# Optimization experiments

Measured on AMD Instinct MI355X. Metric: run time of the kernel, lower is better.

## Reference

```python
import jax, jax.numpy as jnp
import numpy as np

D_MODEL = 1024
N_HEAD = 16
D_HEAD = D_MODEL // N_HEAD


def setup_inputs() -> dict:
    key = jax.random.key(0)
    ks = jax.random.split(key, 12)
    L, B, M = 2048, 2, 2048
    s = 1.0 / np.sqrt(D_MODEL)
    return {
        "q": jax.random.normal(ks[0], (L, B, D_MODEL), jnp.float32),
        "kv": jax.random.normal(ks[1], (L, B, D_MODEL), jnp.float32),
        "mem": jax.random.normal(ks[2], (M, B, D_MODEL), jnp.float32),
        "w_q": jax.random.normal(ks[3], (D_MODEL, D_MODEL), jnp.float32) * s,
        "b_q": jnp.zeros((D_MODEL,), jnp.float32),
        "w_k": jax.random.normal(ks[4], (D_MODEL, D_MODEL), jnp.float32) * s,
        "b_k": jnp.zeros((D_MODEL,), jnp.float32),
        "w_v": jax.random.normal(ks[5], (D_MODEL, D_MODEL), jnp.float32) * s,
        "b_v": jnp.zeros((D_MODEL,), jnp.float32),
        "w_c": jax.random.normal(ks[6], (D_MODEL, D_MODEL), jnp.float32) * s,
        "b_c": jnp.zeros((D_MODEL,), jnp.float32),
    }


def reference(q, kv, mem, w_q, b_q, w_k, b_k, w_v, b_v, w_c, b_c):
    # c: [L+M, B, D]
    c = jnp.concatenate([mem, kv], axis=0)
    L, B, _ = q.shape
    J = c.shape[0]
    # linear projections (torch Linear: x @ W^T + b)
    qh = (q @ w_q.T + b_q).reshape(L, B, N_HEAD, D_HEAD)
    kh = (c @ w_k.T + b_k).reshape(J, B, N_HEAD, D_HEAD)
    vh = (c @ w_v.T + b_v).reshape(J, B, N_HEAD, D_HEAD)
    # attention scores [i, j, b, n]
    score = jnp.einsum("ibnd,jbnd->ijbn", qh, kh) / np.sqrt(D_HEAD).astype(np.float32)
    prob = jax.nn.softmax(score, axis=1)
    vec = jnp.einsum("ijbn,jbnd->ibnd", prob, vh).reshape(L, B, D_MODEL)
    return vec @ w_c.T + b_c
```

## Files before the change

### kernel.cpp

```cpp
#include <hip/hip_runtime.h>


using short8 = __attribute__((ext_vector_type(8))) short;
using f32x4  = __attribute__((ext_vector_type(4))) float;

#define DEV __device__ __forceinline__

DEV unsigned short f2bf(float f) {
  union { float f; unsigned int u; } x; x.f = f;
  unsigned int r = x.u + 0x7FFFu + ((x.u >> 16) & 1u);
  return (unsigned short)(r >> 16);
}

DEV unsigned int cvtpk(float lo, float hi) {
  unsigned int r;
  asm("v_cvt_pk_bf16_f32 %0, %1, %2" : "=v"(r) : "v"(lo), "v"(hi));
  return r;
}

DEV float max3f(float a, float b, float c) {
  float d;
  asm("v_max3_f32 %0, %1, %2, %3" : "=v"(d) : "v"(a), "v"(b), "v"(c));
  return d;
}

DEV void gload_lds16(const unsigned short* g, unsigned short* l) {
  __builtin_amdgcn_global_load_lds(
      (const __attribute__((address_space(1))) unsigned int*)g,
      (__attribute__((address_space(3))) unsigned int*)l, 16, 0, 0);
}

#define BARRIER_RAW()                      \
  do {                                     \
    __builtin_amdgcn_sched_barrier(0);     \
    __builtin_amdgcn_s_barrier();          \
    __builtin_amdgcn_sched_barrier(0);     \
  } while (0)

__global__ __launch_bounds__(256) void convert_all(
    const float* __restrict__ q, const float* __restrict__ mem_,
    const float* __restrict__ kv, const float* __restrict__ wq,
    const float* __restrict__ wk, const float* __restrict__ wv,
    const float* __restrict__ wc, unsigned short* __restrict__ a_bf,
    unsigned short* __restrict__ c_bf, unsigned short* __restrict__ w_bf) {
  size_t u = (size_t)blockIdx.x * 256 + threadIdx.x;
  const float* src;
  unsigned short* dst;
  if (u < 524288u)        { src = q    + u * 8;                dst = a_bf + u * 8; }
  else if (u < 1048576u)  { src = mem_ + (u - 524288u) * 8;    dst = c_bf + (u - 524288u) * 8; }
  else if (u < 1572864u)  { src = kv   + (u - 1048576u) * 8;   dst = c_bf + 4194304u + (u - 1048576u) * 8; }
  else if (u < 1703936u)  { src = wq   + (u - 1572864u) * 8;   dst = w_bf + (u - 1572864u) * 8; }
  else if (u < 1835008u)  { src = wk   + (u - 1703936u) * 8;   dst = w_bf + 1048576u + (u - 1703936u) * 8; }
  else if (u < 1966080u)  { src = wv   + (u - 1835008u) * 8;   dst = w_bf + 2097152u + (u - 1835008u) * 8; }
  else                    { src = wc   + (u - 1966080u) * 8;   dst = w_bf + 3145728u + (u - 1966080u) * 8; }
  float4 v0 = ((const float4*)src)[0];
  float4 v1 = ((const float4*)src)[1];
  union { unsigned short us[8]; uint4 v; } o;
  o.us[0] = f2bf(v0.x); o.us[1] = f2bf(v0.y); o.us[2] = f2bf(v0.z); o.us[3] = f2bf(v0.w);
  o.us[4] = f2bf(v1.x); o.us[5] = f2bf(v1.y); o.us[6] = f2bf(v1.z); o.us[7] = f2bf(v1.w);
  *(uint4*)dst = o.v;
}

template <int MODE>
__global__ __launch_bounds__(256, 2) void gemm_bt(
    const unsigned short* __restrict__ A, const unsigned short* __restrict__ Bw,
    const float* __restrict__ bias, void* __restrict__ outp) {
  __shared__ __align__(16) unsigned short lA[128 * 64];
  __shared__ __align__(16) unsigned short lB[128 * 64];
  const int tid = threadIdx.x;
  const int lane = tid & 63;
  const int w = tid >> 6;
  const int wr = w >> 1, wcn = w & 1;
  const int tm = blockIdx.x * 128;
  const int tn = blockIdx.y * 128;

  const int srow = lane >> 3;
  const int scol = ((lane & 7) ^ srow) * 8;
  const unsigned short* aptr = A + (size_t)(tm + 32 * w + srow) * 1024 + scol;
  const unsigned short* bptr = Bw + (size_t)(tn + 32 * w + srow) * 1024 + scol;
  unsigned short* lAw = &lA[(32 * w) * 64];
  unsigned short* lBw = &lB[(32 * w) * 64];

  const f32x4 zero = {0.f, 0.f, 0.f, 0.f};
  f32x4 acc[4][4];
#pragma unroll
  for (int i = 0; i < 4; ++i)
#pragma unroll
    for (int j = 0; j < 4; ++j) acc[i][j] = zero;

  for (int kb = 0; kb < 16; ++kb) {
    const int ko = kb * 64;
#pragma unroll
    for (int c = 0; c < 4; ++c) {
      gload_lds16(aptr + ko + c * 8 * 1024, lAw + c * 8 * 64);
      gload_lds16(bptr + ko + c * 8 * 1024, lBw + c * 8 * 64);
    }
    __syncthreads();
#pragma unroll
    for (int kk = 0; kk < 2; ++kk) {
      short8 af[4], bfr[4];
#pragma unroll
      for (int mi = 0; mi < 4; ++mi) {
        int r = 64 * wr + 16 * mi + (lane & 15);
        int slot = (kk * 4 + (lane >> 4)) ^ (r & 7);
        af[mi] = *(const short8*)&lA[r * 64 + slot * 8];
      }
#pragma unroll
      for (int ni = 0; ni < 4; ++ni) {
        int r = 64 * wcn + 16 * ni + (lane & 15);
        int slot = (kk * 4 + (lane >> 4)) ^ (r & 7);
        bfr[ni] = *(const short8*)&lB[r * 64 + slot * 8];
      }
#pragma unroll
      for (int mi = 0; mi < 4; ++mi)
#pragma unroll
        for (int ni = 0; ni < 4; ++ni)
          acc[mi][ni] = __builtin_amdgcn_mfma_f32_16x16x32_bf16(
              af[mi], bfr[ni], acc[mi][ni], 0, 0, 0);
    }
    __syncthreads();
  }

  const int g4 = (lane >> 4) * 4;
  const int c0 = lane & 15;
#pragma unroll
  for (int mi = 0; mi < 4; ++mi) {
#pragma unroll
    for (int ni = 0; ni < 4; ++ni) {
      const int colt = tn + 64 * wcn + 16 * ni + c0;
      const float bv = bias[colt];
#pragma unroll
      for (int j = 0; j < 4; ++j) {
        const int rowt = tm + 64 * wr + 16 * mi + g4 + j;
        const float v = acc[mi][ni][j] + bv;
        if constexpr (MODE == 0) {
          ((float*)outp)[(size_t)rowt * 1024 + colt] = v;
        } else if constexpr (MODE == 1) {
          const int i = rowt >> 1, b = rowt & 1, n = colt >> 6, d = colt & 63;
          ((unsigned short*)outp)[(((size_t)(b * 16 + n) * 2048 + i) << 6) + d] =
              f2bf(v * 0.1803368801111f);
        } else if constexpr (MODE == 2) {
          const int jj = rowt >> 1, b = rowt & 1, n = colt >> 6, d = colt & 63;
          ((unsigned short*)outp)[(((size_t)(b * 16 + n) * 4096 + jj) << 6) + d] = f2bf(v);
        } else {
          const int jj = rowt >> 1, b = rowt & 1, n = colt >> 6, d = colt & 63;
          const int j6 = jj & 63;
          const int pos = (j6 & 3) | (((j6 >> 4) & 1) << 2) | (((j6 >> 2) & 3) << 3) |
                          (((j6 >> 5) & 1) << 5);
          ((unsigned short*)outp)[((size_t)(b * 16 + n) * 64 + d) * 4096 + (jj & ~63) + pos] =
              f2bf(v);
        }
      }
    }
  }
}

__global__ __launch_bounds__(256, 2) void attn_kernel(
    const unsigned short* __restrict__ qh, const unsigned short* __restrict__ kh,
    const unsigned short* __restrict__ vt, unsigned short* __restrict__ vec) {
  __shared__ __align__(16) unsigned short kl[2][2][64 * 64];
  __shared__ __align__(16) unsigned short vl[2][2][64 * 64];
  const int tid = threadIdx.x;
  const int lane = tid & 63;
  const int w = tid >> 6;
  const int g = lane >> 4;
  const int l4 = lane & 15;
  const int f = blockIdx.x;
  const int head = (f & 7) * 4 + ((f >> 3) & 3);
  const int qt = f >> 5;
  const int b = head >> 4, n = head & 15;
  const unsigned short* qbase = qh + ((size_t)head * 2048 + qt * 128 + 32 * w) * 64;
  const unsigned short* kbase = kh + (size_t)head * 4096 * 64;
  const unsigned short* vbase = vt + (size_t)head * 64 * 4096;

  short8 qf[2][2];
#pragma unroll
  for (int mi = 0; mi < 2; ++mi)
#pragma unroll
    for (int kk = 0; kk < 2; ++kk)
      qf[mi][kk] = *(const short8*)&qbase[(16 * mi + l4) * 64 + kk * 32 + g * 8];

  const f32x4 zero = {0.f, 0.f, 0.f, 0.f};
  f32x4 oacc[2][4];
#pragma unroll
  for (int mi = 0; mi < 2; ++mi)
#pragma unroll
    for (int nd = 0; nd < 4; ++nd) oacc[mi][nd] = zero;
  float mrow[2] = {-3.0e38f, -3.0e38f};
  float lsum[2] = {0.f, 0.f};

  const int srow = lane >> 3;
  const int scol = ((lane & 7) ^ srow) * 8;
  const unsigned short* kp = kbase + (size_t)(16 * w + srow) * 64 + scol;
  const unsigned short* vp = vbase + (size_t)(16 * w + srow) * 4096 + scol;

  auto stage_pair = [&](int jp, int bufi) {
#pragma unroll
    for (int sub = 0; sub < 2; ++sub) {
      gload_lds16(kp + (size_t)jp * 8192 + sub * 4096,
                  &kl[bufi][sub][(16 * w) * 64]);
      gload_lds16(kp + (size_t)jp * 8192 + sub * 4096 + 8 * 64,
                  &kl[bufi][sub][(16 * w + 8) * 64]);
      gload_lds16(vp + jp * 128 + sub * 64, &vl[bufi][sub][(16 * w) * 64]);
      gload_lds16(vp + jp * 128 + sub * 64 + 8 * 4096,
                  &vl[bufi][sub][(16 * w + 8) * 64]);
    }
  };

  auto subtile = [&](const unsigned short* kbuf, const unsigned short* vbuf) {
    f32x4 s[2][4];
#pragma unroll
    for (int mi = 0; mi < 2; ++mi)
#pragma unroll
      for (int nj = 0; nj < 4; ++nj) s[mi][nj] = zero;
    __builtin_amdgcn_s_setprio(1);
#pragma unroll
    for (int kk = 0; kk < 2; ++kk) {
      short8 bk[4];
#pragma unroll
      for (int nj = 0; nj < 4; ++nj) {
        int r = 16 * nj + l4;
        int slot = (kk * 4 + g) ^ (r & 7);
        bk[nj] = *(const short8*)&kbuf[r * 64 + slot * 8];
      }
#pragma unroll
      for (int mi = 0; mi < 2; ++mi)
#pragma unroll
        for (int nj = 0; nj < 4; ++nj)
          s[mi][nj] = __builtin_amdgcn_mfma_f32_16x16x32_bf16(bk[nj], qf[mi][kk], s[mi][nj], 0, 0, 0);
    }
    __builtin_amdgcn_s_setprio(0);

    float pm[2];
#pragma unroll
    for (int mi = 0; mi < 2; ++mi) {
      float t0 = max3f(s[mi][0][0], s[mi][0][1], s[mi][0][2]);
      float t1 = max3f(s[mi][0][3], s[mi][1][0], s[mi][1][1]);
      float t2 = max3f(s[mi][1][2], s[mi][1][3], s[mi][2][0]);
      float t3 = max3f(s[mi][2][1], s[mi][2][2], s[mi][2][3]);
      float t4 = max3f(s[mi][3][0], s[mi][3][1], s[mi][3][2]);
      float p5 = max3f(t0, t1, t2);
      p5 = max3f(p5, t3, t4);
      pm[mi] = fmaxf(p5, s[mi][3][3]);
    }
    float pj = fmaxf(pm[0], pm[1]);
    pj = fmaxf(pj, __shfl_xor(pj, 16));
    pj = fmaxf(pj, __shfl_xor(pj, 32));
    if (!__all(pj <= fminf(mrow[0], mrow[1]) + 8.f)) {
#pragma unroll
      for (int mi = 0; mi < 2; ++mi) {
        const float mnew = fmaxf(mrow[mi], pj);
        const float sc = __builtin_amdgcn_exp2f(mrow[mi] - mnew);
        mrow[mi] = mnew;
        lsum[mi] *= sc;
#pragma unroll
        for (int reg = 0; reg < 4; ++reg) {
          const float scr = __shfl(sc, 4 * g + reg);
#pragma unroll
          for (int nd = 0; nd < 4; ++nd) oacc[mi][nd][reg] *= scr;
        }
      }
    }

    short8 pa[2][2];
#pragma unroll
    for (int mi = 0; mi < 2; ++mi) {
      const float m = mrow[mi];
      float rs = 0.f;
#pragma unroll
      for (int nj = 0; nj < 4; ++nj)
#pragma unroll
        for (int reg = 0; reg < 4; ++reg) {
          const float p = __builtin_amdgcn_exp2f(s[mi][nj][reg] - m);
          s[mi][nj][reg] = p;
          rs += p;
        }
      lsum[mi] += rs;
#pragma unroll
      for (int kk2 = 0; kk2 < 2; ++kk2) {
        union { unsigned int u[4]; short8 v; } t;
#pragma unroll
        for (int wd = 0; wd < 4; ++wd) {
          const int nj = (wd >> 1) + 2 * kk2;
          const int r0 = (wd & 1) * 2;
          t.u[wd] = cvtpk(s[mi][nj][r0], s[mi][nj][r0 + 1]);
        }
        pa[mi][kk2] = t.v;
      }
    }

    __builtin_amdgcn_s_setprio(1);
#pragma unroll
    for (int kk2 = 0; kk2 < 2; ++kk2) {
      short8 bv4[4];
#pragma unroll
      for (int nd = 0; nd < 4; ++nd) {
        const int r = 16 * nd + l4;
        const int blk = (g + 4 * kk2) ^ (r & 7);
        bv4[nd] = *(const short8*)&vbuf[r * 64 + blk * 8];
      }
#pragma unroll
      for (int mi = 0; mi < 2; ++mi)
#pragma unroll
        for (int nd = 0; nd < 4; ++nd)
          oacc[mi][nd] = __builtin_amdgcn_mfma_f32_16x16x32_bf16(pa[mi][kk2], bv4[nd], oacc[mi][nd], 0, 0, 0);
    }
    __builtin_amdgcn_s_setprio(0);
  };

  stage_pair(0, 0);
  asm volatile("s_waitcnt vmcnt(0)" ::: "memory");
  BARRIER_RAW();

  for (int t2 = 0; t2 < 16; ++t2) {
    stage_pair(2 * t2 + 1, 1);
    subtile(kl[0][0], vl[0][0]);
    subtile(kl[0][1], vl[0][1]);
    asm volatile("s_waitcnt vmcnt(0)" ::: "memory");
    BARRIER_RAW();
    if (t2 < 15) stage_pair(2 * t2 + 2, 0);
    subtile(kl[1][0], vl[1][0]);
    subtile(kl[1][1], vl[1][1]);
    if (t2 < 15) {
      asm volatile("s_waitcnt vmcnt(0)" ::: "memory");
      BARRIER_RAW();
    }
  }

#pragma unroll
  for (int mi = 0; mi < 2; ++mi) {
    float l = lsum[mi];
    l += __shfl_xor(l, 16);
    l += __shfl_xor(l, 32);
#pragma unroll
    for (int reg = 0; reg < 4; ++reg) {
      const float lr = __shfl(l, 4 * g + reg);
      const float inv = 1.f / lr;
      const int i = qt * 128 + 32 * w + 16 * mi + 4 * g + reg;
#pragma unroll
      for (int nd = 0; nd < 4; ++nd) {
        const int d = 16 * nd + l4;
        vec[(size_t)(i * 2 + b) * 1024 + n * 64 + d] = f2bf(oacc[mi][nd][reg] * inv);
      }
    }
  }
}

extern "C" void kernel_launch(void* const* d_in, const int* in_sizes, int n_in,
                              void* d_out, int out_size, void* d_ws, size_t ws_size,
                              hipStream_t stream) {
  (void)in_sizes; (void)n_in; (void)out_size; (void)ws_size;
  const float* q    = (const float*)d_in[0];
  const float* kv   = (const float*)d_in[1];
  const float* mem_ = (const float*)d_in[2];
  const float* wq   = (const float*)d_in[3];
  const float* bq   = (const float*)d_in[4];
  const float* wk   = (const float*)d_in[5];
  const float* bk   = (const float*)d_in[6];
  const float* wv   = (const float*)d_in[7];
  const float* bv   = (const float*)d_in[8];
  const float* wc   = (const float*)d_in[9];
  const float* bc   = (const float*)d_in[10];

  char* ws = (char*)d_ws;
  unsigned short* w_bf = (unsigned short*)(ws);
  unsigned short* a_bf = (unsigned short*)(ws + (8ull << 20));
  unsigned short* c_bf = (unsigned short*)(ws + (16ull << 20));
  unsigned short* qhb  = (unsigned short*)(ws + (32ull << 20));
  unsigned short* khb  = (unsigned short*)(ws + (40ull << 20));
  unsigned short* vtb  = (unsigned short*)(ws + (56ull << 20));
  unsigned short* vecb = a_bf;

  convert_all<<<8192, 256, 0, stream>>>(q, mem_, kv, wq, wk, wv, wc, a_bf, c_bf, w_bf);
  gemm_bt<1><<<dim3(32, 8), 256, 0, stream>>>(a_bf, w_bf,                bq, qhb);
  gemm_bt<2><<<dim3(64, 8), 256, 0, stream>>>(c_bf, w_bf + (1u << 20),   bk, khb);
  gemm_bt<3><<<dim3(64, 8), 256, 0, stream>>>(c_bf, w_bf + (2u << 20),   bv, vtb);
  attn_kernel<<<512, 256, 0, stream>>>(qhb, khb, vtb, vecb);
  gemm_bt<0><<<dim3(32, 8), 256, 0, stream>>>(vecb, w_bf + (3u << 20),   bc, d_out);
}
```

Before: 189.6 us.

## Split attention over two key halves and merge partials in a combine kernel

The attention kernel now splits the 4096 keys of each head into two halves, doubling the grid to 1024 blocks and raising the launch-bounds occupancy target to 4 blocks per CU with half the LDS staging. Each block writes a normalized partial output plus its row max and row sum. A new combine kernel rescales and merges the two partials into the final layout. This is meant to improve latency hiding and CU occupancy, at the cost of an extra launch and extra global traffic for the partial outputs.

```diff
diff --git a/kernel.cpp b/kernel.cpp
--- a/kernel.cpp
+++ b/kernel.cpp
@@ -10,6 +10,12 @@
   union { float f; unsigned int u; } x; x.f = f;
   unsigned int r = x.u + 0x7FFFu + ((x.u >> 16) & 1u);
   return (unsigned short)(r >> 16);
+}
+
+DEV float bf2f(unsigned short u) {
+  union { unsigned int u; float f; } x;
+  x.u = ((unsigned int)u) << 16;
+  return x.f;
 }
 
 DEV unsigned int cvtpk(float lo, float hi) {
@@ -155,20 +161,21 @@
   }
 }
 
-__global__ __launch_bounds__(256, 2) void attn_kernel(
+__global__ __launch_bounds__(256, 4) void attn_kernel(
     const unsigned short* __restrict__ qh, const unsigned short* __restrict__ kh,
-    const unsigned short* __restrict__ vt, unsigned short* __restrict__ vec) {
-  __shared__ __align__(16) unsigned short kl[2][2][64 * 64];
-  __shared__ __align__(16) unsigned short vl[2][2][64 * 64];
+    const unsigned short* __restrict__ vt, unsigned short* __restrict__ po,
+    float2* __restrict__ ml) {
+  __shared__ __align__(16) unsigned short kl[2][64 * 64];
+  __shared__ __align__(16) unsigned short vl[2][64 * 64];
   const int tid = threadIdx.x;
   const int lane = tid & 63;
   const int w = tid >> 6;
   const int g = lane >> 4;
   const int l4 = lane & 15;
   const int f = blockIdx.x;
-  const int head = (f & 7) * 4 + ((f >> 3) & 3);
-  const int qt = f >> 5;
-  const int b = head >> 4, n = head & 15;
+  const int head = (f & 7) * 4 + (f >> 8);
+  const int qt = (f >> 3) & 15;
+  const int half = (f >> 7) & 1;
   const unsigned short* qbase = qh + ((size_t)head * 2048 + qt * 128 + 32 * w) * 64;
   const unsigned short* kbase = kh + (size_t)head * 4096 * 64;
   const unsigned short* vbase = vt + (size_t)head * 64 * 4096;
@@ -193,18 +200,14 @@
   const int scol = ((lane & 7) ^ srow) * 8;
   const unsigned short* kp = kbase + (size_t)(16 * w + srow) * 64 + scol;
   const unsigned short* vp = vbase + (size_t)(16 * w + srow) * 4096 + scol;
-
-  auto stage_pair = [&](int jp, int bufi) {
-#pragma unroll
-    for (int sub = 0; sub < 2; ++sub) {
-      gload_lds16(kp + (size_t)jp * 8192 + sub * 4096,
-                  &kl[bufi][sub][(16 * w) * 64]);
-      gload_lds16(kp + (size_t)jp * 8192 + sub * 4096 + 8 * 64,
-                  &kl[bufi][sub][(16 * w + 8) * 64]);
-      gload_lds16(vp + jp * 128 + sub * 64, &vl[bufi][sub][(16 * w) * 64]);
-      gload_lds16(vp + jp * 128 + sub * 64 + 8 * 4096,
-                  &vl[bufi][sub][(16 * w + 8) * 64]);
-    }
+  const int stbase = half * 32;
+
+  auto stage = [&](int st, int bufi) {
+    const size_t jt = (size_t)(stbase + st);
+    gload_lds16(kp + jt * 4096,            &kl[bufi][(16 * w) * 64]);
+    gload_lds16(kp + jt * 4096 + 8 * 64,   &kl[bufi][(16 * w + 8) * 64]);
+    gload_lds16(vp + jt * 64,              &vl[bufi][(16 * w) * 64]);
+    gload_lds16(vp + jt * 64 + 8 * 4096,   &vl[bufi][(16 * w + 8) * 64]);
   };
 
   auto subtile = [&](const unsigned short* kbuf, const unsigned short* vbuf) {
@@ -308,19 +311,17 @@
     __builtin_amdgcn_s_setprio(0);
   };
 
-  stage_pair(0, 0);
+  stage(0, 0);
   asm volatile("s_waitcnt vmcnt(0)" ::: "memory");
   BARRIER_RAW();
 
   for (int t2 = 0; t2 < 16; ++t2) {
-    stage_pair(2 * t2 + 1, 1);
-    subtile(kl[0][0], vl[0][0]);
-    subtile(kl[0][1], vl[0][1]);
+    stage(2 * t2 + 1, 1);
+    subtile(kl[0], vl[0]);
     asm volatile("s_waitcnt vmcnt(0)" ::: "memory");
     BARRIER_RAW();
-    if (t2 < 15) stage_pair(2 * t2 + 2, 0);
-    subtile(kl[1][0], vl[1][0]);
-    subtile(kl[1][1], vl[1][1]);
+    if (t2 < 15) stage(2 * t2 + 2, 0);
+    subtile(kl[1], vl[1]);
     if (t2 < 15) {
       asm volatile("s_waitcnt vmcnt(0)" ::: "memory");
       BARRIER_RAW();
@@ -332,18 +333,48 @@
     float l = lsum[mi];
     l += __shfl_xor(l, 16);
     l += __shfl_xor(l, 32);
+    const int rowbase = head * 2048 + qt * 128 + 32 * w + 16 * mi;
+    if (g == 0)
+      ml[(size_t)half * 65536 + rowbase + l4] = make_float2(mrow[mi], l);
 #pragma unroll
     for (int reg = 0; reg < 4; ++reg) {
       const float lr = __shfl(l, 4 * g + reg);
       const float inv = 1.f / lr;
-      const int i = qt * 128 + 32 * w + 16 * mi + 4 * g + reg;
+      const size_t row = rowbase + 4 * g + reg;
 #pragma unroll
       for (int nd = 0; nd < 4; ++nd) {
         const int d = 16 * nd + l4;
-        vec[(size_t)(i * 2 + b) * 1024 + n * 64 + d] = f2bf(oacc[mi][nd][reg] * inv);
+        po[(size_t)half * 4194304 + row * 64 + d] = f2bf(oacc[mi][nd][reg] * inv);
       }
     }
   }
+}
+
+__global__ __launch_bounds__(256) void attn_combine(
+    const unsigned short* __restrict__ po, const float2* __restrict__ ml,
+    unsigned short* __restrict__ vec) {
+  const size_t u = (size_t)blockIdx.x * 256 + threadIdx.x;
+  const size_t row = u >> 3;
+  const int d0 = (int)(u & 7) * 8;
+  const int head = (int)(row >> 11);
+  const int i = (int)(row & 2047);
+  const int b = head >> 4, n = head & 15;
+
+  const float2 m0 = ml[row];
+  const float2 m1 = ml[65536 + row];
+  const float m = fmaxf(m0.x, m1.x);
+  const float w0 = m0.y * __builtin_amdgcn_exp2f(m0.x - m);
+  const float w1 = m1.y * __builtin_amdgcn_exp2f(m1.x - m);
+  const float inv = 1.f / (w0 + w1);
+  const float a0 = w0 * inv, a1 = w1 * inv;
+
+  union { uint4 v; unsigned short us[8]; } p0, p1, o;
+  p0.v = *(const uint4*)&po[row * 64 + d0];
+  p1.v = *(const uint4*)&po[4194304 + row * 64 + d0];
+#pragma unroll
+  for (int k = 0; k < 8; ++k)
+    o.us[k] = f2bf(bf2f(p0.us[k]) * a0 + bf2f(p1.us[k]) * a1);
+  *(uint4*)&vec[(size_t)(i * 2 + b) * 1024 + n * 64 + d0] = o.v;
 }
 
 extern "C" void kernel_launch(void* const* d_in, const int* in_sizes, int n_in,
@@ -370,11 +401,14 @@
   unsigned short* khb  = (unsigned short*)(ws + (40ull << 20));
   unsigned short* vtb  = (unsigned short*)(ws + (56ull << 20));
   unsigned short* vecb = a_bf;
+  unsigned short* po   = c_bf;
+  float2*         ml   = (float2*)ws;
 
   convert_all<<<8192, 256, 0, stream>>>(q, mem_, kv, wq, wk, wv, wc, a_bf, c_bf, w_bf);
   gemm_bt<1><<<dim3(32, 8), 256, 0, stream>>>(a_bf, w_bf,                bq, qhb);
   gemm_bt<2><<<dim3(64, 8), 256, 0, stream>>>(c_bf, w_bf + (1u << 20),   bk, khb);
   gemm_bt<3><<<dim3(64, 8), 256, 0, stream>>>(c_bf, w_bf + (2u << 20),   bv, vtb);
-  attn_kernel<<<512, 256, 0, stream>>>(qhb, khb, vtb, vecb);
+  attn_kernel<<<1024, 256, 0, stream>>>(qhb, khb, vtb, po, ml);
+  attn_combine<<<2048, 256, 0, stream>>>(po, ml, vecb);
   gemm_bt<0><<<dim3(32, 8), 256, 0, stream>>>(vecb, w_bf + (3u << 20),   bc, d_out);
 }
```

Measured after the change: 204.4 us. 1.08x slower.

## Merge K/V projection launches and interleave two QK^T subtiles in attention

Applied to the files above, without the earlier changes.

Replaces the separate K and V projection GEMM launches with a single gemm_kv kernel on a 64x16 grid, where the y index selects the weight, bias and output layout. This removes one launch and the tail of a 512-block grid. The attention loop now issues both QK^T MFMA subtiles before their softmax and PV stages, so the second subtile's matrix work can overlap the first's exp/softmax, at the cost of more live registers. The row-sum reduction is also reshaped into a pairwise tree to shorten the dependency chain.

```diff
diff --git a/kernel.cpp b/kernel.cpp
--- a/kernel.cpp
+++ b/kernel.cpp
@@ -135,20 +135,101 @@
         const float v = acc[mi][ni][j] + bv;
         if constexpr (MODE == 0) {
           ((float*)outp)[(size_t)rowt * 1024 + colt] = v;
-        } else if constexpr (MODE == 1) {
+        } else {
           const int i = rowt >> 1, b = rowt & 1, n = colt >> 6, d = colt & 63;
           ((unsigned short*)outp)[(((size_t)(b * 16 + n) * 2048 + i) << 6) + d] =
               f2bf(v * 0.1803368801111f);
-        } else if constexpr (MODE == 2) {
-          const int jj = rowt >> 1, b = rowt & 1, n = colt >> 6, d = colt & 63;
-          ((unsigned short*)outp)[(((size_t)(b * 16 + n) * 4096 + jj) << 6) + d] = f2bf(v);
+        }
+      }
+    }
+  }
+}
+
+__global__ __launch_bounds__(256, 2) void gemm_kv(
+    const unsigned short* __restrict__ A, const unsigned short* __restrict__ wk,
+    const unsigned short* __restrict__ wv, const float* __restrict__ bk,
+    const float* __restrict__ bv, unsigned short* __restrict__ ko,
+    unsigned short* __restrict__ vo) {
+  __shared__ __align__(16) unsigned short lA[128 * 64];
+  __shared__ __align__(16) unsigned short lB[128 * 64];
+  const int tid = threadIdx.x;
+  const int lane = tid & 63;
+  const int w = tid >> 6;
+  const int wr = w >> 1, wcn = w & 1;
+  const int tm = blockIdx.x * 128;
+  const int yy = blockIdx.y;
+  const bool isV = yy >= 8;
+  const int tn = (yy & 7) * 128;
+  const unsigned short* Bw = isV ? wv : wk;
+  const float* bias = isV ? bv : bk;
+
+  const int srow = lane >> 3;
+  const int scol = ((lane & 7) ^ srow) * 8;
+  const unsigned short* aptr = A + (size_t)(tm + 32 * w + srow) * 1024 + scol;
+  const unsigned short* bptr = Bw + (size_t)(tn + 32 * w + srow) * 1024 + scol;
+  unsigned short* lAw = &lA[(32 * w) * 64];
+  unsigned short* lBw = &lB[(32 * w) * 64];
+
+  const f32x4 zero = {0.f, 0.f, 0.f, 0.f};
+  f32x4 acc[4][4];
+#pragma unroll
+  for (int i = 0; i < 4; ++i)
+#pragma unroll
+    for (int j = 0; j < 4; ++j) acc[i][j] = zero;
+
+  for (int kb = 0; kb < 16; ++kb) {
+    const int ko_ = kb * 64;
+#pragma unroll
+    for (int c = 0; c < 4; ++c) {
+      gload_lds16(aptr + ko_ + c * 8 * 1024, lAw + c * 8 * 64);
+      gload_lds16(bptr + ko_ + c * 8 * 1024, lBw + c * 8 * 64);
+    }
+    __syncthreads();
+#pragma unroll
+    for (int kk = 0; kk < 2; ++kk) {
+      short8 af[4], bfr[4];
+#pragma unroll
+      for (int mi = 0; mi < 4; ++mi) {
+        int r = 64 * wr + 16 * mi + (lane & 15);
+        int slot = (kk * 4 + (lane >> 4)) ^ (r & 7);
+        af[mi] = *(const short8*)&lA[r * 64 + slot * 8];
+      }
+#pragma unroll
+      for (int ni = 0; ni < 4; ++ni) {
+        int r = 64 * wcn + 16 * ni + (lane & 15);
+        int slot = (kk * 4 + (lane >> 4)) ^ (r & 7);
+        bfr[ni] = *(const short8*)&lB[r * 64 + slot * 8];
+      }
+#pragma unroll
+      for (int mi = 0; mi < 4; ++mi)
+#pragma unroll
+        for (int ni = 0; ni < 4; ++ni)
+          acc[mi][ni] = __builtin_amdgcn_mfma_f32_16x16x32_bf16(
+              af[mi], bfr[ni], acc[mi][ni], 0, 0, 0);
+    }
+    __syncthreads();
+  }
+
+  const int g4 = (lane >> 4) * 4;
+  const int c0 = lane & 15;
+#pragma unroll
+  for (int mi = 0; mi < 4; ++mi) {
+#pragma unroll
+    for (int ni = 0; ni < 4; ++ni) {
+      const int colt = tn + 64 * wcn + 16 * ni + c0;
+      const float bvv = bias[colt];
+#pragma unroll
+      for (int j = 0; j < 4; ++j) {
+        const int rowt = tm + 64 * wr + 16 * mi + g4 + j;
+        const float v = acc[mi][ni][j] + bvv;
+        const int jj = rowt >> 1, b = rowt & 1, n = colt >> 6, d = colt & 63;
+        if (!isV) {
+          ko[(((size_t)(b * 16 + n) * 4096 + jj) << 6) + d] = f2bf(v);
         } else {
-          const int jj = rowt >> 1, b = rowt & 1, n = colt >> 6, d = colt & 63;
           const int j6 = jj & 63;
           const int pos = (j6 & 3) | (((j6 >> 4) & 1) << 2) | (((j6 >> 2) & 3) << 3) |
                           (((j6 >> 5) & 1) << 5);
-          ((unsigned short*)outp)[((size_t)(b * 16 + n) * 64 + d) * 4096 + (jj & ~63) + pos] =
-              f2bf(v);
+          vo[((size_t)(b * 16 + n) * 64 + d) * 4096 + (jj & ~63) + pos] = f2bf(v);
         }
       }
     }
@@ -207,8 +288,7 @@
     }
   };
 
-  auto subtile = [&](const unsigned short* kbuf, const unsigned short* vbuf) {
-    f32x4 s[2][4];
+  auto qkt = [&](const unsigned short* kbuf, f32x4 (&s)[2][4]) {
 #pragma unroll
     for (int mi = 0; mi < 2; ++mi)
 #pragma unroll
@@ -230,7 +310,9 @@
           s[mi][nj] = __builtin_amdgcn_mfma_f32_16x16x32_bf16(bk[nj], qf[mi][kk], s[mi][nj], 0, 0, 0);
     }
     __builtin_amdgcn_s_setprio(0);
-
+  };
+
+  auto sm = [&](f32x4 (&s)[2][4], short8 (&pa)[2][2]) {
     float pm[2];
 #pragma unroll
     for (int mi = 0; mi < 2; ++mi) {
@@ -261,21 +343,20 @@
         }
       }
     }
-
-    short8 pa[2][2];
 #pragma unroll
     for (int mi = 0; mi < 2; ++mi) {
       const float m = mrow[mi];
-      float rs = 0.f;
-#pragma unroll
-      for (int nj = 0; nj < 4; ++nj)
-#pragma unroll
-        for (int reg = 0; reg < 4; ++reg) {
-          const float p = __builtin_amdgcn_exp2f(s[mi][nj][reg] - m);
-          s[mi][nj][reg] = p;
-          rs += p;
-        }
-      lsum[mi] += rs;
+      float tr[4];
+#pragma unroll
+      for (int nj = 0; nj < 4; ++nj) {
+        const float p0 = __builtin_amdgcn_exp2f(s[mi][nj][0] - m);
+        const float p1 = __builtin_amdgcn_exp2f(s[mi][nj][1] - m);
+        const float p2 = __builtin_amdgcn_exp2f(s[mi][nj][2] - m);
+        const float p3 = __builtin_amdgcn_exp2f(s[mi][nj][3] - m);
+        s[mi][nj][0] = p0; s[mi][nj][1] = p1; s[mi][nj][2] = p2; s[mi][nj][3] = p3;
+        tr[nj] = (p0 + p1) + (p2 + p3);
+      }
+      lsum[mi] += (tr[0] + tr[1]) + (tr[2] + tr[3]);
 #pragma unroll
       for (int kk2 = 0; kk2 < 2; ++kk2) {
         union { unsigned int u[4]; short8 v; } t;
@@ -288,7 +369,9 @@
         pa[mi][kk2] = t.v;
       }
     }
-
+  };
+
+  auto pv = [&](const short8 (&pa)[2][2], const unsigned short* vbuf) {
     __builtin_amdgcn_s_setprio(1);
 #pragma unroll
     for (int kk2 = 0; kk2 < 2; ++kk2) {
@@ -308,19 +391,28 @@
     __builtin_amdgcn_s_setprio(0);
   };
 
+  f32x4 sA[2][4], sB[2][4];
+  short8 paA[2][2], paB[2][2];
+  auto pair = [&](int bufi) {
+    qkt(kl[bufi][0], sA);
+    qkt(kl[bufi][1], sB);
+    sm(sA, paA);
+    pv(paA, vl[bufi][0]);
+    sm(sB, paB);
+    pv(paB, vl[bufi][1]);
+  };
+
   stage_pair(0, 0);
   asm volatile("s_waitcnt vmcnt(0)" ::: "memory");
   BARRIER_RAW();
 
   for (int t2 = 0; t2 < 16; ++t2) {
     stage_pair(2 * t2 + 1, 1);
-    subtile(kl[0][0], vl[0][0]);
-    subtile(kl[0][1], vl[0][1]);
+    pair(0);
     asm volatile("s_waitcnt vmcnt(0)" ::: "memory");
     BARRIER_RAW();
     if (t2 < 15) stage_pair(2 * t2 + 2, 0);
-    subtile(kl[1][0], vl[1][0]);
-    subtile(kl[1][1], vl[1][1]);
+    pair(1);
     if (t2 < 15) {
       asm volatile("s_waitcnt vmcnt(0)" ::: "memory");
       BARRIER_RAW();
@@ -372,9 +464,9 @@
   unsigned short* vecb = a_bf;
 
   convert_all<<<8192, 256, 0, stream>>>(q, mem_, kv, wq, wk, wv, wc, a_bf, c_bf, w_bf);
-  gemm_bt<1><<<dim3(32, 8), 256, 0, stream>>>(a_bf, w_bf,                bq, qhb);
-  gemm_bt<2><<<dim3(64, 8), 256, 0, stream>>>(c_bf, w_bf + (1u << 20),   bk, khb);
-  gemm_bt<3><<<dim3(64, 8), 256, 0, stream>>>(c_bf, w_bf + (2u << 20),   bv, vtb);
+  gemm_bt<1><<<dim3(32, 8), 256, 0, stream>>>(a_bf, w_bf, bq, qhb);
+  gemm_kv<<<dim3(64, 16), 256, 0, stream>>>(c_bf, w_bf + (1u << 20), w_bf + (2u << 20),
+                                            bk, bv, khb, vtb);
   attn_kernel<<<512, 256, 0, stream>>>(qhb, khb, vtb, vecb);
-  gemm_bt<0><<<dim3(32, 8), 256, 0, stream>>>(vecb, w_bf + (3u << 20),   bc, d_out);
-}
+  gemm_bt<0><<<dim3(32, 8), 256, 0, stream>>>(vecb, w_bf + (3u << 20), bc, d_out);
+}
```

New measurement: 180.9 us. 4.6% less time.
